# Performance work log

Hardware: AMD Instinct MI355X
Metric: run time of the kernel (lower is better)

The kernel has to match this reference:

```python
import jax, jax.numpy as jnp
import numpy as np
from itertools import combinations_with_replacement

KSIZE = 13  # 1 + 6*int(start_scale) with start_scale=2.0 (fixed at init)


def gaussian_kernel3d(scale):
    # torch: sigma = max(0.1, min(sigma, 10)); kernel detached (requires_grad=False)
    sigma = jnp.clip(jax.lax.stop_gradient(scale), 0.1, 10.0)
    k1 = jnp.arange(KSIZE, dtype=jnp.float32) - KSIZE // 2
    k1 = jnp.exp(-(k1 ** 2) / (2.0 * sigma ** 2))
    k3 = jnp.einsum('i,j,k->ijk', k1, k1, k1)
    return k3 / k3.sum()


def blur3d(vol, kernel):
    # replicate ('edge') padding then VALID conv, matching padding_mode='replicate'
    p = KSIZE // 2
    vp = jnp.pad(vol, ((0, 0), (0, 0), (p, p), (p, p), (p, p)), mode='edge')
    w = kernel[None, None]  # [O=1, I=1, kD, kH, kW]
    return jax.lax.conv_general_dilated(
        vp, w, window_strides=(1, 1, 1), padding='VALID',
        dimension_numbers=('NCDHW', 'OIDHW', 'NCDHW'))


def tgrad(f, axis):
    # torch.gradient: central diff interior, one-sided first-order at edges
    n = f.shape[axis]
    sl = lambda a, b: jax.lax.slice_in_dim(f, a, b, axis=axis)
    interior = (sl(2, n) - sl(0, n - 2)) * 0.5
    first = sl(1, 2) - sl(0, 1)
    last = sl(n - 1, n) - sl(n - 2, n - 1)
    return jnp.concatenate([first, interior, last], axis=axis)


def setup_inputs() -> dict:
    key = jax.random.key(0)
    kx, k1, k2, k3, k4 = jax.random.split(key, 5)
    B, D, H, W = 2, 128, 128, 128
    x = jax.random.normal(kx, (B, 1, D, H, W), dtype=jnp.float32)
    scale = jnp.asarray(2.0, dtype=jnp.float32)
    # Linear(7,10) and Linear(10,1), torch layout [out, in]
    lim1 = 1.0 / np.sqrt(7.0)
    lim2 = 1.0 / np.sqrt(10.0)
    W1 = jax.random.uniform(k1, (10, 7), jnp.float32, -lim1, lim1)
    b1 = jax.random.uniform(k2, (10,), jnp.float32, -lim1, lim1)
    W2 = jax.random.uniform(k3, (1, 10), jnp.float32, -lim2, lim2)
    b2 = jax.random.uniform(k4, (1,), jnp.float32, -lim2, lim2)
    return {'x': x, 'scale': scale, 'W1': W1, 'b1': b1, 'W2': W2, 'b2': b2}


def reference(x, scale, W1, b1, W2, b2):
    B = x.shape[0]
    D, H, W = x.shape[2], x.shape[3], x.shape[4]
    smoothed = blur3d(x, gaussian_kernel3d(scale))  # [B,1,D,H,W]
    axes = [2, 3, 4]
    g = [tgrad(smoothed, a) for a in axes]
    H_elems = [tgrad(g[a0 - 2], a1) for a0, a1 in combinations_with_replacement(axes, 2)]
    h = jnp.stack(H_elems)                      # [6,B,1,D,H,W]
    h = jnp.moveaxis(h, 0, -1)                  # [B,1,D,H,W,6]
    h = h.reshape(B, D * H * W, 6)              # flatten dims 1..4 (C=1)
    scale_col = jnp.broadcast_to(scale, (B, D * H * W, 1))
    feat = jnp.concatenate([h, scale_col], axis=2)  # [B,N,7]
    hid = jax.nn.relu(feat @ W1.T + b1)             # [B,N,10]
    out = jax.nn.sigmoid(hid @ W2.T + b2)           # [B,N,1]
    out = out.reshape(B, D, H, W, 1)
    return jnp.transpose(out, (0, 4, 1, 2, 3))      # [B,1,D,H,W]
```

## Files before the change

kernel.cpp:

```cpp
#include <hip/hip_runtime.h>
#include <math.h>

#define NVOX (2 * 128 * 128 * 128)
#define KS 13
#define KR 6
#define LROWS 44

__device__ __forceinline__ float4 LD4(const float* p) {
    return *reinterpret_cast<const float4*>(p);
}

__device__ __forceinline__ void make_weights(float scale, float* wv) {
    float sig = fminf(fmaxf(scale, 0.1f), 10.0f);
    float inv2s2 = -1.0f / (2.0f * sig * sig);
    float sum = 0.f;
#pragma unroll
    for (int t = 0; t < KS; ++t) {
        float d = (float)(t - KR);
        wv[t] = __expf(d * d * inv2s2);
        sum += wv[t];
    }
    float r = 1.0f / sum;
#pragma unroll
    for (int t = 0; t < KS; ++t) wv[t] *= r;
}

__global__ __launch_bounds__(256) void wh_blur_kernel(const float* __restrict__ in,
                                                      float* __restrict__ out,
                                                      const float* __restrict__ scale_p) {
    __shared__ float T[LROWS * 128];
    const int i = blockIdx.x;
    const int wid = ((i & 7) << 7) | (i >> 3);
    const int slice = wid >> 2;
    const int h0 = (wid & 3) << 5;
    const float* sp = in + (slice << 14);
    float* op = out + (slice << 14);

    float wv[KS];
    make_weights(scale_p[0], wv);

    for (int it = 0; it < 6; ++it) {
        int g = threadIdx.x + (it << 8);
        if (g < LROWS * 32) {
            int w0 = (g & 31) << 2;
            int lr = g >> 5;
            int r = h0 - 6 + lr;
            r = r < 0 ? 0 : (r > 127 ? 127 : r);
            const float* rp = sp + (r << 7);

            float F[20];
            if (w0 >= 8 && w0 <= 116) {
                float4 q0 = LD4(rp + w0 - 8), q1 = LD4(rp + w0 - 4), q2 = LD4(rp + w0),
                       q3 = LD4(rp + w0 + 4), q4 = LD4(rp + w0 + 8);
                F[0] = q0.x; F[1] = q0.y; F[2] = q0.z; F[3] = q0.w;
                F[4] = q1.x; F[5] = q1.y; F[6] = q1.z; F[7] = q1.w;
                F[8] = q2.x; F[9] = q2.y; F[10] = q2.z; F[11] = q2.w;
                F[12] = q3.x; F[13] = q3.y; F[14] = q3.z; F[15] = q3.w;
                F[16] = q4.x; F[17] = q4.y; F[18] = q4.z; F[19] = q4.w;
            } else {
#pragma unroll
                for (int i2 = 0; i2 < 16; ++i2) {
                    int ww = w0 - 6 + i2;
                    ww = ww < 0 ? 0 : (ww > 127 ? 127 : ww);
                    F[i2 + 2] = rp[ww];
                }
            }
            float a0 = 0.f, a1 = 0.f, a2 = 0.f, a3 = 0.f;
#pragma unroll
            for (int t = 0; t < KS; ++t) {
                float wt = wv[t];
                a0 = fmaf(wt, F[2 + t], a0);
                a1 = fmaf(wt, F[3 + t], a1);
                a2 = fmaf(wt, F[4 + t], a2);
                a3 = fmaf(wt, F[5 + t], a3);
            }
            *reinterpret_cast<float4*>(&T[(lr << 7) + w0]) = make_float4(a0, a1, a2, a3);
        }
    }
    __syncthreads();

    {
        const int w0 = (threadIdx.x & 31) << 2;
        const int r0 = (threadIdx.x >> 5) << 2;

        float4 win[KS];
#pragma unroll
        for (int t = 0; t < KS; ++t) win[t] = LD4(&T[((r0 + t) << 7) + w0]);
#pragma unroll
        for (int s = 0; s < 4; ++s) {
            float4 acc = make_float4(0.f, 0.f, 0.f, 0.f);
#pragma unroll
            for (int t = 0; t < KS; ++t) {
                float4 v = win[(s + t) % KS];
                float wt = wv[t];
                acc.x = fmaf(wt, v.x, acc.x);
                acc.y = fmaf(wt, v.y, acc.y);
                acc.z = fmaf(wt, v.z, acc.z);
                acc.w = fmaf(wt, v.w, acc.w);
            }
            *reinterpret_cast<float4*>(op + ((h0 + r0 + s) << 7) + w0) = acc;
            int nl = r0 + s + 13;
            nl = nl > LROWS - 1 ? LROWS - 1 : nl;
            win[s % KS] = LD4(&T[(nl << 7) + w0]);
        }
    }
}

__global__ __launch_bounds__(256) void dblur_kernel(const float* __restrict__ in,
                                                    float* __restrict__ out,
                                                    const float* __restrict__ scale_p) {
    const int i = blockIdx.x;
    const int wid = ((i & 7) << 6) | (i >> 3);
    const int t0 = wid * 256 + threadIdx.x;
    const int w0 = (t0 & 31) << 2;
    const int h  = (t0 >> 5) & 127;
    const int d0 = ((t0 >> 12) & 15) << 3;
    const int b  = t0 >> 16;
    const int base = (b << 21) | (h << 7) | w0;

    float wv[KS];
    make_weights(scale_p[0], wv);

    float4 win[KS];
#pragma unroll
    for (int t = 0; t < KS; ++t) {
        int r = d0 - 6 + t;
        r = r < 0 ? 0 : (r > 127 ? 127 : r);
        win[t] = LD4(in + base + (r << 14));
    }
#pragma unroll
    for (int s = 0; s < 8; ++s) {
        float4 acc = make_float4(0.f, 0.f, 0.f, 0.f);
#pragma unroll
        for (int t = 0; t < KS; ++t) {
            float4 v = win[(s + t) % KS];
            float wt = wv[t];
            acc.x = fmaf(wt, v.x, acc.x);
            acc.y = fmaf(wt, v.y, acc.y);
            acc.z = fmaf(wt, v.z, acc.z);
            acc.w = fmaf(wt, v.w, acc.w);
        }
        *reinterpret_cast<float4*>(out + base + ((d0 + s) << 14)) = acc;
        int rn = d0 + s + 7;
        rn = rn > 127 ? 127 : rn;
        win[s % KS] = LD4(in + base + (rn << 14));
    }
}

__device__ __forceinline__ void lohi(int c, int& lo, int& hi, float& s) {
    lo = c > 0 ? c - 1 : 0;
    hi = c < 127 ? c + 1 : 127;
    s = 1.0f / (float)(hi - lo);
}

__device__ __forceinline__ int CH(int v) {
    return v < 0 ? 0 : (v > 127 ? 127 : v);
}

__global__ __launch_bounds__(256) void hess_mlp_kernel(const float* __restrict__ S,
                                const float* __restrict__ scale_p,
                                const float* __restrict__ W1, const float* __restrict__ b1,
                                const float* __restrict__ W2, const float* __restrict__ b2,
                                float* __restrict__ out) {
    const int i = blockIdx.x;
    const int wid = ((i & 7) << 7) | (i >> 3);
    const int t = wid * 256 + threadIdx.x;
    const int l = t & 31;
    const int w0 = l << 2;
    const int hb = ((t >> 5) & 31) << 2;
    const int d = (t >> 10) & 127;
    const int b = t >> 17;
    const int lane = threadIdx.x & 63;
    const bool l0 = (l == 0), l31 = (l == 31);

    int ld, hd; float sd; lohi(d, ld, hd, sd);
    int ti, tj; float s_hd, s_ld;
    lohi(hd, ti, tj, s_hd); lohi(ld, ti, tj, s_ld);
    const bool d_top = (d == 127), d_bot = (d == 0);
    const int dp2 = d > 125 ? 127 : d + 2;
    const int dm2 = d < 2 ? 0 : d - 2;

    float sw[4], s_hw[4], s_lw[4];
#pragma unroll
    for (int j = 0; j < 4; ++j) {
        int lw, hw; lohi(w0 + j, lw, hw, sw[j]);
        lohi(hw, ti, tj, s_hw[j]); lohi(lw, ti, tj, s_lw[j]);
    }

    const float scale = scale_p[0];
    float b1e[10];
#pragma unroll
    for (int u = 0; u < 10; ++u) b1e[u] = fmaf(scale, W1[u * 7 + 6], b1[u]);

    const float* base = S + (b << 21) + w0;
    auto RP = [&](int dd, int hh) { return base + (dd << 14) + (hh << 7); };
    float* obase = out + (b << 21) + (d << 14) + w0;

    float4 nd0 = LD4(RP(d, CH(hb - 2))), nd1 = LD4(RP(d, CH(hb - 1))),
           nd2 = LD4(RP(d, hb)),        nd3 = LD4(RP(d, hb + 1)),
           nd4 = LD4(RP(d, CH(hb + 2)));
    float4 pm0 = LD4(RP(ld, CH(hb - 1))), pm1 = LD4(RP(ld, hb)), pm2 = LD4(RP(ld, hb + 1));
    float4 pp0 = LD4(RP(hd, CH(hb - 1))), pp1 = LD4(RP(hd, hb)), pp2 = LD4(RP(hd, hb + 1));

#pragma unroll
    for (int s = 0; s < 4; ++s) {
        const int h = hb + s;
        const float4 qp = LD4(RP(dp2, h));
        const float4 qm = LD4(RP(dm2, h));

        int lh, hh; float sh; lohi(h, lh, hh, sh);
        float s_hh, s_lh; lohi(hh, ti, tj, s_hh); lohi(lh, ti, tj, s_lh);
        const bool h_top = (h == 127), h_bot = (h == 0);

        float c_lz = __shfl(nd2.z, lane - 1), c_lw = __shfl(nd2.w, lane - 1);
        float c_rx = __shfl(nd2.x, lane + 1), c_ry = __shfl(nd2.y, lane + 1);
        float r1_lw = __shfl(nd1.w, lane - 1), r1_rx = __shfl(nd1.x, lane + 1);
        float r3_lw = __shfl(nd3.w, lane - 1), r3_rx = __shfl(nd3.x, lane + 1);
        float pmlw = __shfl(pm1.w, lane - 1), pmrx = __shfl(pm1.x, lane + 1);
        float pplw = __shfl(pp1.w, lane - 1), pprx = __shfl(pp1.x, lane + 1);

        const float va[4]  = {nd2.x, nd2.y, nd2.z, nd2.w};
        const float n0a[4] = {nd0.x, nd0.y, nd0.z, nd0.w};
        const float n1a[4] = {nd1.x, nd1.y, nd1.z, nd1.w};
        const float n3a[4] = {nd3.x, nd3.y, nd3.z, nd3.w};
        const float n4a[4] = {nd4.x, nd4.y, nd4.z, nd4.w};
        const float pm0a[4] = {pm0.x, pm0.y, pm0.z, pm0.w};
        const float pm1a[4] = {pm1.x, pm1.y, pm1.z, pm1.w};
        const float pm2a[4] = {pm2.x, pm2.y, pm2.z, pm2.w};
        const float pp0a[4] = {pp0.x, pp0.y, pp0.z, pp0.w};
        const float pp1a[4] = {pp1.x, pp1.y, pp1.z, pp1.w};
        const float pp2a[4] = {pp2.x, pp2.y, pp2.z, pp2.w};
        const float qpa[4] = {qp.x, qp.y, qp.z, qp.w};
        const float qma[4] = {qm.x, qm.y, qm.z, qm.w};

        const float c_m1[4] = {l0 ? va[0] : c_lw, va[0], va[1], va[2]};
        const float c_p1[4] = {va[1], va[2], va[3], l31 ? va[3] : c_rx};
        const float c_m2[4] = {l0 ? va[0] : c_lz, l0 ? va[0] : c_lw, va[0], va[1]};
        const float c_p2[4] = {va[2], va[3], l31 ? va[3] : c_rx, l31 ? va[3] : c_ry};
        const float r1m[4] = {l0 ? n1a[0] : r1_lw, n1a[0], n1a[1], n1a[2]};
        const float r1p[4] = {n1a[1], n1a[2], n1a[3], l31 ? n1a[3] : r1_rx};
        const float r3m[4] = {l0 ? n3a[0] : r3_lw, n3a[0], n3a[1], n3a[2]};
        const float r3p[4] = {n3a[1], n3a[2], n3a[3], l31 ? n3a[3] : r3_rx};
        const float pmm[4] = {l0 ? pm1a[0] : pmlw, pm1a[0], pm1a[1], pm1a[2]};
        const float pmp[4] = {pm1a[1], pm1a[2], pm1a[3], l31 ? pm1a[3] : pmrx};
        const float ppm[4] = {l0 ? pp1a[0] : pplw, pp1a[0], pp1a[1], pp1a[2]};
        const float ppp[4] = {pp1a[1], pp1a[2], pp1a[3], l31 ? pp1a[3] : pprx};

        float ov[4];
#pragma unroll
        for (int j = 0; j < 4; ++j) {
            const float fDD = sd * (s_hd * (qpa[j] - (d_top ? pm1a[j] : va[j]))
                                  - s_ld * ((d_bot ? pp1a[j] : va[j]) - qma[j]));
            const float fHH = sh * (s_hh * (n4a[j] - (h_top ? n1a[j] : va[j]))
                                  - s_lh * ((h_bot ? n3a[j] : va[j]) - n0a[j]));
            const float fDH = sd * sh * ((pp2a[j] - pp0a[j]) - (pm2a[j] - pm0a[j]));
            const float fHW = sh * sw[j] * ((r3p[j] - r3m[j]) - (r1p[j] - r1m[j]));
            const float fDW = sd * sw[j] * ((ppp[j] - ppm[j]) - (pmp[j] - pmm[j]));
            const float Aw = (j == 3 && l31) ? c_m1[j] : va[j];
            const float Bw = (j == 0 && l0) ? c_p1[j] : va[j];
            const float fWW = sw[j] * (s_hw[j] * (c_p2[j] - Aw) - s_lw[j] * (Bw - c_m2[j]));

            const float ft[6] = {fDD, fDH, fDW, fHH, fHW, fWW};
            float o = b2[0];
#pragma unroll
            for (int u = 0; u < 10; ++u) {
                float a = b1e[u];
#pragma unroll
                for (int k = 0; k < 6; ++k) a = fmaf(ft[k], W1[u * 7 + k], a);
                a = fmaxf(a, 0.f);
                o = fmaf(a, W2[u], o);
            }
            float e = __expf(-o);
            ov[j] = __builtin_amdgcn_rcpf(1.0f + e);
        }
        *reinterpret_cast<float4*>(obase + (h << 7)) = make_float4(ov[0], ov[1], ov[2], ov[3]);

        nd0 = nd1; nd1 = nd2; nd2 = nd3; nd3 = nd4;
        nd4 = LD4(RP(d, CH(h + 3)));
        pm0 = pm1; pm1 = pm2; pm2 = LD4(RP(ld, CH(h + 2)));
        pp0 = pp1; pp1 = pp2; pp2 = LD4(RP(hd, CH(h + 2)));
    }
}

extern "C" void kernel_launch(void* const* d_in, const int* in_sizes, int n_in,
                              void* d_out, int out_size, void* d_ws, size_t ws_size,
                              hipStream_t stream) {
    const float* x     = (const float*)d_in[0];
    const float* scale = (const float*)d_in[1];
    const float* W1    = (const float*)d_in[2];
    const float* b1    = (const float*)d_in[3];
    const float* W2    = (const float*)d_in[4];
    const float* b2    = (const float*)d_in[5];
    float* out = (float*)d_out;

    float* ws0 = (float*)d_ws;
    float* ws1 = ws0 + NVOX;

    wh_blur_kernel<<<2 * 128 * 4, 256, 0, stream>>>(x, ws1, scale);
    dblur_kernel<<<NVOX / 32 / 256, 256, 0, stream>>>(ws1, ws0, scale);
    hess_mlp_kernel<<<NVOX / 16 / 256, 256, 0, stream>>>(ws0, scale, W1, b1, W2, b2, out);
}
```

Measured before the change: 47.40 us.

## Widen per-thread W-blur outputs and double H rows per Hessian thread

The W-direction blur now has each thread compute 16 outputs from 36 loaded values (9 float4 loads) instead of 4 outputs from 20, with explicit replicate-edge handling for the first and last segments. This cuts the redundant halo loads and per-thread loop overhead. The Hessian/MLP kernel now processes 8 H rows per thread instead of 4, halving the grid and reusing the sliding neighbor registers across more rows. Both changes raise register pressure and lower thread count, which may reduce occupancy.

```diff
diff --git a/kernel.cpp b/kernel.cpp
--- a/kernel.cpp
+++ b/kernel.cpp
@@ -39,42 +39,59 @@
     float wv[KS];
     make_weights(scale_p[0], wv);
 
-    for (int it = 0; it < 6; ++it) {
+    for (int it = 0; it < 2; ++it) {
         int g = threadIdx.x + (it << 8);
-        if (g < LROWS * 32) {
-            int w0 = (g & 31) << 2;
-            int lr = g >> 5;
+        if (g < LROWS * 8) {
+            int wseg = g & 7;
+            int w0 = wseg << 4;
+            int lr = g >> 3;
             int r = h0 - 6 + lr;
             r = r < 0 ? 0 : (r > 127 ? 127 : r);
             const float* rp = sp + (r << 7);
 
-            float F[20];
-            if (w0 >= 8 && w0 <= 116) {
-                float4 q0 = LD4(rp + w0 - 8), q1 = LD4(rp + w0 - 4), q2 = LD4(rp + w0),
-                       q3 = LD4(rp + w0 + 4), q4 = LD4(rp + w0 + 8);
-                F[0] = q0.x; F[1] = q0.y; F[2] = q0.z; F[3] = q0.w;
-                F[4] = q1.x; F[5] = q1.y; F[6] = q1.z; F[7] = q1.w;
-                F[8] = q2.x; F[9] = q2.y; F[10] = q2.z; F[11] = q2.w;
-                F[12] = q3.x; F[13] = q3.y; F[14] = q3.z; F[15] = q3.w;
-                F[16] = q4.x; F[17] = q4.y; F[18] = q4.z; F[19] = q4.w;
+            float F[36];
+            if (wseg >= 1 && wseg <= 6) {
+#pragma unroll
+                for (int i2 = 0; i2 < 9; ++i2) {
+                    float4 q = LD4(rp + w0 - 8 + (i2 << 2));
+                    F[4 * i2] = q.x; F[4 * i2 + 1] = q.y;
+                    F[4 * i2 + 2] = q.z; F[4 * i2 + 3] = q.w;
+                }
+            } else if (wseg == 0) {
+                float e = rp[0];
+#pragma unroll
+                for (int i2 = 0; i2 < 8; ++i2) F[i2] = e;
+#pragma unroll
+                for (int i2 = 0; i2 < 7; ++i2) {
+                    float4 q = LD4(rp + (i2 << 2));
+                    F[8 + 4 * i2] = q.x; F[9 + 4 * i2] = q.y;
+                    F[10 + 4 * i2] = q.z; F[11 + 4 * i2] = q.w;
+                }
             } else {
-#pragma unroll
-                for (int i2 = 0; i2 < 16; ++i2) {
-                    int ww = w0 - 6 + i2;
-                    ww = ww < 0 ? 0 : (ww > 127 ? 127 : ww);
-                    F[i2 + 2] = rp[ww];
+                float e = rp[127];
+#pragma unroll
+                for (int i2 = 0; i2 < 6; ++i2) {
+                    float4 q = LD4(rp + 104 + (i2 << 2));
+                    F[4 * i2] = q.x; F[4 * i2 + 1] = q.y;
+                    F[4 * i2 + 2] = q.z; F[4 * i2 + 3] = q.w;
                 }
+#pragma unroll
+                for (int i2 = 24; i2 < 36; ++i2) F[i2] = e;
             }
-            float a0 = 0.f, a1 = 0.f, a2 = 0.f, a3 = 0.f;
+
+            float a[16];
+#pragma unroll
+            for (int k = 0; k < 16; ++k) a[k] = 0.f;
 #pragma unroll
             for (int t = 0; t < KS; ++t) {
                 float wt = wv[t];
-                a0 = fmaf(wt, F[2 + t], a0);
-                a1 = fmaf(wt, F[3 + t], a1);
-                a2 = fmaf(wt, F[4 + t], a2);
-                a3 = fmaf(wt, F[5 + t], a3);
+#pragma unroll
+                for (int k = 0; k < 16; ++k) a[k] = fmaf(wt, F[k + 2 + t], a[k]);
             }
-            *reinterpret_cast<float4*>(&T[(lr << 7) + w0]) = make_float4(a0, a1, a2, a3);
+#pragma unroll
+            for (int k = 0; k < 4; ++k)
+                *reinterpret_cast<float4*>(&T[(lr << 7) + w0 + (k << 2)]) =
+                    make_float4(a[4 * k], a[4 * k + 1], a[4 * k + 2], a[4 * k + 3]);
         }
     }
     __syncthreads();
@@ -163,13 +180,13 @@
                                 const float* __restrict__ W2, const float* __restrict__ b2,
                                 float* __restrict__ out) {
     const int i = blockIdx.x;
-    const int wid = ((i & 7) << 7) | (i >> 3);
+    const int wid = ((i & 7) << 6) | (i >> 3);
     const int t = wid * 256 + threadIdx.x;
     const int l = t & 31;
     const int w0 = l << 2;
-    const int hb = ((t >> 5) & 31) << 2;
-    const int d = (t >> 10) & 127;
-    const int b = t >> 17;
+    const int hb = ((t >> 5) & 15) << 3;
+    const int d = (t >> 9) & 127;
+    const int b = t >> 16;
     const int lane = threadIdx.x & 63;
     const bool l0 = (l == 0), l31 = (l == 31);
 
@@ -198,12 +215,12 @@
 
     float4 nd0 = LD4(RP(d, CH(hb - 2))), nd1 = LD4(RP(d, CH(hb - 1))),
            nd2 = LD4(RP(d, hb)),        nd3 = LD4(RP(d, hb + 1)),
-           nd4 = LD4(RP(d, CH(hb + 2)));
+           nd4 = LD4(RP(d, hb + 2));
     float4 pm0 = LD4(RP(ld, CH(hb - 1))), pm1 = LD4(RP(ld, hb)), pm2 = LD4(RP(ld, hb + 1));
     float4 pp0 = LD4(RP(hd, CH(hb - 1))), pp1 = LD4(RP(hd, hb)), pp2 = LD4(RP(hd, hb + 1));
 
 #pragma unroll
-    for (int s = 0; s < 4; ++s) {
+    for (int s = 0; s < 8; ++s) {
         const int h = hb + s;
         const float4 qp = LD4(RP(dp2, h));
         const float4 qm = LD4(RP(dm2, h));
@@ -298,5 +315,5 @@
 
     wh_blur_kernel<<<2 * 128 * 4, 256, 0, stream>>>(x, ws1, scale);
     dblur_kernel<<<NVOX / 32 / 256, 256, 0, stream>>>(ws1, ws0, scale);
-    hess_mlp_kernel<<<NVOX / 16 / 256, 256, 0, stream>>>(ws0, scale, W1, b1, W2, b2, out);
-}
+    hess_mlp_kernel<<<NVOX / 32 / 256, 256, 0, stream>>>(ws0, scale, W1, b1, W2, b2, out);
+}
```

Measured after the change: 52.05 us. +9.8%, slower.
